# Performance work log

Hardware: AMD Instinct MI355X
Metric: run time of the kernel (lower is better)

## Reference

```python
import jax, jax.numpy as jnp
import numpy as np
from jax import lax

K_NEIGHBORS = 8  # num_neighbors
EPS_BN = 1e-5

def _bn(x, g, b, axes):
    # training-mode batch norm over `axes`, channel axis = 1
    m = jnp.mean(x, axis=axes, keepdims=True)
    v = jnp.var(x, axis=axes, keepdims=True)
    shp = [1] * x.ndim; shp[1] = x.shape[1]
    return (x - m) / jnp.sqrt(v + EPS_BN) * g.reshape(shp) + b.reshape(shp)

def _conv(x, w, b):
    y = lax.conv_general_dilated(x, w, (1, 1), 'SAME',
                                 dimension_numbers=('NCHW', 'OIHW', 'NCHW'))
    return y + b[None, :, None, None]

def setup_inputs() -> dict:
    key = jax.random.key(0)
    ks = jax.random.split(key, 20)
    B, C, H, W = 64, 200, 27, 27
    D, F, NC, HID = 64, 9, 16, 128
    inp = {
        'x': jax.random.normal(ks[0], (B, C, H, W), jnp.float32),
        'conv1_w': jax.random.normal(ks[1], (32, C, 3, 3), jnp.float32) * 0.02,
        'conv1_b': jnp.zeros((32,), jnp.float32),
        'bn1_g': jnp.ones((32,), jnp.float32), 'bn1_b': jnp.zeros((32,), jnp.float32),
        'conv2_w': jax.random.normal(ks[2], (64, 32, 3, 3), jnp.float32) * 0.05,
        'conv2_b': jnp.zeros((64,), jnp.float32),
        'bn2_g': jnp.ones((64,), jnp.float32), 'bn2_b': jnp.zeros((64,), jnp.float32),
        'conv3_w': jax.random.normal(ks[3], (D, 64, 3, 3), jnp.float32) * 0.05,
        'conv3_b': jnp.zeros((D,), jnp.float32),
        'bn3_g': jnp.ones((D,), jnp.float32), 'bn3_b': jnp.zeros((D,), jnp.float32),
        'w_self': jax.random.normal(ks[4], (D, D), jnp.float32) * (2.0 / (2 * D)) ** 0.5,
        'w_nb': jax.random.normal(ks[5], (D, D), jnp.float32) * (2.0 / (2 * D)) ** 0.5,
        'gkan_bias': jnp.zeros((D,), jnp.float32),
        'kan_a': jax.random.normal(ks[6], (D, 3), jnp.float32) * 0.1,
        'kan_b': jax.random.normal(ks[7], (D, 2), jnp.float32) * 0.1,
        'gkan_bn_g': jnp.ones((D,), jnp.float32), 'gkan_bn_b': jnp.zeros((D,), jnp.float32),
        'centers': jax.random.normal(ks[8], (D, F), jnp.float32),
        'gamma': jnp.ones((D, F), jnp.float32) * 0.5,
        'attn_w1': jax.random.normal(ks[9], (D // 4, D), jnp.float32) * 0.1,
        'attn_b1': jnp.zeros((D // 4,), jnp.float32),
        'attn_w2': jax.random.normal(ks[10], (D, D // 4), jnp.float32) * 0.1,
        'attn_b2': jnp.zeros((D,), jnp.float32),
        'fa_bn_g': jnp.ones((D,), jnp.float32), 'fa_bn_b': jnp.zeros((D,), jnp.float32),
        'fc1_w': jax.random.normal(ks[11], (HID, D), jnp.float32) * 0.1,
        'fc1_b': jnp.zeros((HID,), jnp.float32),
        'cls_bn_g': jnp.ones((HID,), jnp.float32), 'cls_bn_b': jnp.zeros((HID,), jnp.float32),
        'fc2_w': jax.random.normal(ks[12], (NC, HID), jnp.float32) * 0.1,
        'fc2_b': jnp.zeros((NC,), jnp.float32),
    }
    return inp

def _forward(x, conv1_w, conv1_b, bn1_g, bn1_b, conv2_w, conv2_b, bn2_g, bn2_b,
             conv3_w, conv3_b, bn3_g, bn3_b, w_self, w_nb, gkan_bias, kan_a, kan_b,
             gkan_bn_g, gkan_bn_b, centers, gamma, attn_w1, attn_b1, attn_w2, attn_b2,
             fa_bn_g, fa_bn_b, fc1_w, fc1_b, cls_bn_g, cls_bn_b, fc2_w, fc2_b):
    # --- CNN encoder ---
    h = jax.nn.relu(_bn(_conv(x, conv1_w, conv1_b), bn1_g, bn1_b, (0, 2, 3)))
    h = jax.nn.relu(_bn(_conv(h, conv2_w, conv2_b), bn2_g, bn2_b, (0, 2, 3)))
    h = jax.nn.relu(_bn(_conv(h, conv3_w, conv3_b), bn3_g, bn3_b, (0, 2, 3)))
    # --- tokenize: [B,D,H,W] -> [B,N,D] ---
    B, D, H, W = h.shape
    N = H * W
    t = h.reshape(B, D, N).transpose(0, 2, 1)
    # --- kNN graph (vectorized topk + scatter) ---
    xx = jnp.sum(t * t, axis=-1, keepdims=True)               # [B,N,1]
    xy = jnp.einsum('bnd,bmd->bnm', t, t)                     # [B,N,N]
    dist = jnp.maximum(xx - 2.0 * xy + xx.transpose(0, 2, 1), 0.0)
    k = min(K_NEIGHBORS + 1, N)
    _, idx = lax.top_k(-dist, k)                              # smallest-k, [B,N,k]
    adj = jnp.zeros((B, N, N), t.dtype).at[
        jnp.arange(B)[:, None, None], jnp.arange(N)[None, :, None], idx[:, :, 1:]
    ].set(1.0)
    deg = jnp.sum(adj, axis=-1) + 1e-6                        # [B,N]
    dinv = deg ** -0.5
    adj_norm = dinv[:, :, None] * adj * dinv[:, None, :] + jnp.eye(N, dtype=t.dtype)[None]
    # --- GKAN graph conv ---
    h_self = t @ w_self                                       # [B,N,D]
    h_nb = jnp.einsum('bnm,bmd->bnd', adj_norm, t @ w_nb)
    g = h_self + h_nb + gkan_bias
    g2 = g * g
    num = kan_a[:, 0] + kan_a[:, 1] * g + kan_a[:, 2] * g2
    den = 1.0 + jnp.abs(kan_b[:, 0] * g + kan_b[:, 1] * g2)
    g = num / (den + 1e-8)
    g = _bn(g.transpose(0, 2, 1), gkan_bn_g, gkan_bn_b, (0, 2)).transpose(0, 2, 1)
    # --- Fuzzy attention (RBF membership; logsumexp(log(v+1e-10)) == sum(v+1e-10)) ---
    d2 = (g[..., None] - centers[None, None]) ** 2            # [B,N,D,F]
    rbf = jnp.sum(jnp.exp(-jnp.abs(gamma)[None, None] * d2) + 1e-10, axis=-1)
    a1 = jax.nn.relu(rbf @ attn_w1.T + attn_b1)
    attn = jax.nn.sigmoid(a1 @ attn_w2.T + attn_b2)
    g = g * attn + g
    g = _bn(g.transpose(0, 2, 1), fa_bn_g, fa_bn_b, (0, 2)).transpose(0, 2, 1)
    # dropout: identity in eval
    # --- global pool + classifier ---
    p = 0.5 * jnp.mean(g, axis=1) + 0.5 * jnp.max(g, axis=1)  # [B,D]
    c = p @ fc1_w.T + fc1_b
    c = jax.nn.relu(_bn(c, cls_bn_g, cls_bn_b, (0,)))
    return c @ fc2_w.T + fc2_b

def reference(x, conv1_w, conv1_b, bn1_g, bn1_b, conv2_w, conv2_b, bn2_g, bn2_b,
              conv3_w, conv3_b, bn3_g, bn3_b, w_self, w_nb, gkan_bias, kan_a, kan_b,
              gkan_bn_g, gkan_bn_b, centers, gamma, attn_w1, attn_b1, attn_w2, attn_b2,
              fa_bn_g, fa_bn_b, fc1_w, fc1_b, cls_bn_g, cls_bn_b, fc2_w, fc2_b):
    return _forward(x, conv1_w, conv1_b, bn1_g, bn1_b, conv2_w, conv2_b, bn2_g, bn2_b,
                    conv3_w, conv3_b, bn3_g, bn3_b, w_self, w_nb, gkan_bias, kan_a, kan_b,
                    gkan_bn_g, gkan_bn_b, centers, gamma, attn_w1, attn_b1, attn_w2, attn_b2,
                    fa_bn_g, fa_bn_b, fc1_w, fc1_b, cls_bn_g, cls_bn_b, fc2_w, fc2_b)
```

## Files before the change

### kernel.cpp

```cpp
#include <hip/hip_runtime.h>
#include <math.h>

#define BATCH 64
#define NTOK  729
#define DIM   64
#define NROWS 46656

#define SROW 33
#define SCH  (29 * SROW)

template<int CIN_CHUNK, int TC, bool BN_IN>
__global__ __launch_bounds__(256) void conv3x3_v3(
    const float* __restrict__ in, const float* __restrict__ wgt,
    const float* __restrict__ scsh, float* __restrict__ outp,
    int Cin, int Cout, int cinPerSlab, int nslab)
{
  int groups = Cout / TC;
  int blocksPerB = groups * nslab;
  int b = blockIdx.x / blocksPerB;
  int rr = blockIdx.x % blocksPerB;
  int g = rr / nslab;
  int slab = rr % nslab;
  int c_begin = slab * cinPerSlab;
  int c_end = c_begin + cinPerSlab; if (c_end > Cin) c_end = Cin;

  __shared__ float s_in[CIN_CHUNK * SCH];
  __shared__ float s_w[TC * CIN_CHUNK * 12];
  __shared__ float s_sc[CIN_CHUNK];
  __shared__ float s_sh[CIN_CHUNK];

  const int tid = threadIdx.x;
  const bool active = tid < 243;
  const int py = tid / 9;
  const int px3 = (tid % 9) * 3;

  float acc[TC][3];
  #pragma unroll
  for (int t = 0; t < TC; ++t) { acc[t][0]=0.f; acc[t][1]=0.f; acc[t][2]=0.f; }

  const size_t inB = (size_t)b * Cin;

  for (int c0 = c_begin; c0 < c_end; c0 += CIN_CHUNK) {
    int ccn = c_end - c0; if (ccn > CIN_CHUNK) ccn = CIN_CHUNK;
    if (BN_IN && tid < ccn) {
      s_sc[tid] = scsh[c0 + tid];
      s_sh[tid] = scsh[Cin + c0 + tid];
    }
    __syncthreads();
    for (int i = tid; i < CIN_CHUNK * SCH; i += 256) {
      int cc = i / SCH; int r2 = i - cc * SCH; int y = r2 / SROW; int x2 = r2 - y * SROW;
      float v = 0.f;
      if (cc < ccn && y >= 1 && y <= 27 && x2 >= 1 && x2 <= 27) {
        v = in[(inB + (c0 + cc)) * 729 + (y - 1) * 27 + (x2 - 1)];
        if (BN_IN) v = fmaxf(fmaf(v, s_sc[cc], s_sh[cc]), 0.f);
      }
      s_in[i] = v;
    }
    for (int i = tid; i < TC * CIN_CHUNK * 9; i += 256) {
      int t = i / (CIN_CHUNK * 9); int r2 = i - t * CIN_CHUNK * 9;
      int cc = r2 / 9; int k = r2 - cc * 9;
      float wv = 0.f;
      if (cc < ccn) wv = wgt[((size_t)(g * TC + t) * Cin + (c0 + cc)) * 9 + k];
      s_w[(t * CIN_CHUNK + cc) * 12 + k] = wv;
    }
    __syncthreads();
    if (active) {
      #pragma unroll 1
      for (int cc = 0; cc < ccn; ++cc) {
        const float* bp = &s_in[cc * SCH + py * SROW + px3];
        float v00=bp[0],        v01=bp[1],        v02=bp[2],        v03=bp[3],        v04=bp[4];
        float v10=bp[SROW],     v11=bp[SROW+1],   v12=bp[SROW+2],   v13=bp[SROW+3],   v14=bp[SROW+4];
        float v20=bp[2*SROW],   v21=bp[2*SROW+1], v22=bp[2*SROW+2], v23=bp[2*SROW+3], v24=bp[2*SROW+4];
        #pragma unroll
        for (int t = 0; t < TC; ++t) {
          const float4 wa = *(const float4*)&s_w[(t * CIN_CHUNK + cc) * 12];
          const float4 wb = *(const float4*)&s_w[(t * CIN_CHUNK + cc) * 12 + 4];
          const float  w8 = s_w[(t * CIN_CHUNK + cc) * 12 + 8];
          acc[t][0] += wa.x*v00+wa.y*v01+wa.z*v02 + wa.w*v10+wb.x*v11+wb.y*v12 + wb.z*v20+wb.w*v21+w8*v22;
          acc[t][1] += wa.x*v01+wa.y*v02+wa.z*v03 + wa.w*v11+wb.x*v12+wb.y*v13 + wb.z*v21+wb.w*v22+w8*v23;
          acc[t][2] += wa.x*v02+wa.y*v03+wa.z*v04 + wa.w*v12+wb.x*v13+wb.y*v14 + wb.z*v22+wb.w*v23+w8*v24;
        }
      }
    }
  }
  if (active) {
    #pragma unroll
    for (int t = 0; t < TC; ++t) {
      size_t base = (((size_t)slab * BATCH + b) * Cout + (g * TC + t)) * 729 + py * 27 + px3;
      outp[base+0]=acc[t][0]; outp[base+1]=acc[t][1]; outp[base+2]=acc[t][2];
    }
  }
}

__global__ __launch_bounds__(256) void conv_reduce_stats(
    const float* __restrict__ part, const float* __restrict__ bias,
    float* __restrict__ outp, double* __restrict__ stats, int C, int nslab)
{
  int b = blockIdx.x / C;
  int c = blockIdx.x % C;
  size_t slabStride = (size_t)BATCH * C * 729;
  size_t base = ((size_t)b * C + c) * 729;
  float bv = bias[c];
  float bsum = 0.f, bsq = 0.f;
  for (int e = threadIdx.x; e < 729; e += 256) {
    float v = bv;
    for (int s = 0; s < nslab; ++s) v += part[s*slabStride + base + e];
    outp[base + e] = v;
    bsum += v; bsq += v*v;
  }
  #pragma unroll
  for (int off = 32; off > 0; off >>= 1) {
    bsum += __shfl_down(bsum, off);
    bsq  += __shfl_down(bsq, off);
  }
  __shared__ float rs[4], rq[4];
  int wid = threadIdx.x >> 6;
  if ((threadIdx.x & 63) == 0) { rs[wid] = bsum; rq[wid] = bsq; }
  __syncthreads();
  if (threadIdx.x == 0) {
    float s1 = rs[0]+rs[1]+rs[2]+rs[3];
    float q1 = rq[0]+rq[1]+rq[2]+rq[3];
    atomicAdd(&stats[c], (double)s1);
    atomicAdd(&stats[C + c], (double)q1);
  }
}

__global__ void bn_finalize(const double* __restrict__ stats,
                            const float* __restrict__ gamma, const float* __restrict__ beta,
                            float* __restrict__ scsh, int C, float invCount)
{
  int c = threadIdx.x + blockIdx.x * blockDim.x; if (c >= C) return;
  double mu = stats[c] * (double)invCount;
  double var = stats[C + c] * (double)invCount - mu * mu;
  float rstd = (float)(1.0 / sqrt(var + 1e-5));
  float sc = gamma[c] * rstd;
  scsh[c] = sc;
  scsh[C + c] = beta[c] - (float)mu * sc;
}

__global__ __launch_bounds__(256) void bn_transpose_xx(
    const float* __restrict__ c3, const float* __restrict__ scsh,
    float* __restrict__ t, float* __restrict__ xx)
{
  int lb = (blockIdx.x & 7) * 96 + (blockIdx.x >> 3);
  int b = lb / 12, nt = lb % 12, n0 = nt * 64;
  __shared__ float s[64 * 65];
  for (int i = threadIdx.x; i < 4096; i += 256) {
    int d = i >> 6, j = i & 63; int n = n0 + j;
    float v = 0.f;
    if (n < 729) {
      v = c3[((size_t)b * 64 + d) * 729 + n];
      v = fmaxf(fmaf(v, scsh[d], scsh[64 + d]), 0.f);
    }
    s[d * 65 + j] = v;
  }
  __syncthreads();
  for (int i = threadIdx.x; i < 4096; i += 256) {
    int j = i >> 6, d = i & 63; int n = n0 + j;
    if (n < 729) t[((size_t)b * 729 + n) * 64 + d] = s[d * 65 + j];
  }
  if (threadIdx.x < 64) {
    int j = threadIdx.x; int n = n0 + j;
    if (n < 729) {
      float sm = 0.f;
      #pragma unroll
      for (int d = 0; d < 64; ++d) { float v = s[d * 65 + j]; sm += v * v; }
      xx[b * 729 + n] = sm;
    }
  }
}

__global__ __launch_bounds__(256) void gemm_selfnb(
    const float* __restrict__ t, const float* __restrict__ wself,
    const float* __restrict__ wnb, float* __restrict__ hs, float* __restrict__ hw)
{
  int lb = (blockIdx.x & 7) * 96 + (blockIdx.x >> 3);
  int b = lb / 12, nt = lb % 12, n0 = nt * 64;
  __shared__ __align__(16) float s_tT[64 * 68];
  __shared__ __align__(16) float s_a[64 * 68];
  __shared__ __align__(16) float s_b[64 * 68];
  const int tid = threadIdx.x;
  for (int i = tid; i < 1024; i += 256) {
    int n = i >> 4, dq = i & 15;
    float4 v = make_float4(0.f, 0.f, 0.f, 0.f);
    if (n0 + n < 729) v = *(const float4*)&t[((size_t)b * 729 + n0 + n) * 64 + 4 * dq];
    s_tT[(4*dq+0)*68 + n] = v.x;
    s_tT[(4*dq+1)*68 + n] = v.y;
    s_tT[(4*dq+2)*68 + n] = v.z;
    s_tT[(4*dq+3)*68 + n] = v.w;
  }
  for (int i = tid; i < 1024; i += 256) {
    int d = i >> 4, jq = i & 15;
    *(float4*)&s_a[d*68 + 4*jq] = *(const float4*)&wself[d*64 + 4*jq];
    *(float4*)&s_b[d*68 + 4*jq] = *(const float4*)&wnb[d*64 + 4*jq];
  }
  __syncthreads();
  int ty = tid >> 4, tx = tid & 15;
  float acc0[4][4], acc1[4][4];
  #pragma unroll
  for (int i = 0; i < 4; ++i)
    #pragma unroll
    for (int j = 0; j < 4; ++j) { acc0[i][j] = 0.f; acc1[i][j] = 0.f; }
  #pragma unroll 8
  for (int d = 0; d < 64; ++d) {
    float4 av = *(const float4*)&s_tT[d*68 + 4*ty];
    float4 b1 = *(const float4*)&s_a[d*68 + 4*tx];
    float4 b2 = *(const float4*)&s_b[d*68 + 4*tx];
    float a[4] = {av.x, av.y, av.z, av.w};
    float u[4] = {b1.x, b1.y, b1.z, b1.w};
    float w[4] = {b2.x, b2.y, b2.z, b2.w};
    #pragma unroll
    for (int i = 0; i < 4; ++i)
      #pragma unroll
      for (int j = 0; j < 4; ++j) { acc0[i][j] += a[i]*u[j]; acc1[i][j] += a[i]*w[j]; }
  }
  #pragma unroll
  for (int i = 0; i < 4; ++i) {
    int n = n0 + 4*ty + i;
    if (n < 729) {
      size_t o = ((size_t)b * 729 + n) * 64 + 4*tx;
      *(float4*)&hs[o] = make_float4(acc0[i][0], acc0[i][1], acc0[i][2], acc0[i][3]);
      *(float4*)&hw[o] = make_float4(acc1[i][0], acc1[i][1], acc1[i][2], acc1[i][3]);
    }
  }
}

__global__ __launch_bounds__(256) void dist_topk(
    const float* __restrict__ t, const float* __restrict__ xx, int* __restrict__ nbr)
{
  int lb = (blockIdx.x & 7) * 96 + (blockIdx.x >> 3);
  int b = lb / 12, nt = lb % 12, n0 = nt * 64;
  __shared__ __align__(16) float s_nT[64 * 68];
  __shared__ __align__(16) float s_mT[64 * 68];
  __shared__ __align__(16) float s_S[64 * 68];

  const int tid = threadIdx.x;
  const int ty = tid >> 4, tx = tid & 15;
  const int r = tid & 63, q = tid >> 6;
  const int n_self = n0 + r;
  const size_t tb = (size_t)b * 729;

  float kv[8]; int ki[8];
  #pragma unroll
  for (int i = 0; i < 8; ++i) { kv[i] = 3.0e38f; ki[i] = 0x7fffffff; }

  for (int i = tid; i < 1024; i += 256) {
    int n = i >> 4, dq = i & 15;
    float4 v = make_float4(0.f, 0.f, 0.f, 0.f);
    if (n0 + n < 729) v = *(const float4*)&t[(tb + n0 + n) * 64 + 4 * dq];
    s_nT[(4*dq+0)*68 + n] = v.x;
    s_nT[(4*dq+1)*68 + n] = v.y;
    s_nT[(4*dq+2)*68 + n] = v.z;
    s_nT[(4*dq+3)*68 + n] = v.w;
  }
  for (int i = tid; i < 1024; i += 256) {
    int m = i >> 4, dq = i & 15;
    float4 v = *(const float4*)&t[(tb + m) * 64 + 4 * dq];
    s_mT[(4*dq+0)*68 + m] = v.x;
    s_mT[(4*dq+1)*68 + m] = v.y;
    s_mT[(4*dq+2)*68 + m] = v.z;
    s_mT[(4*dq+3)*68 + m] = v.w;
  }
  __syncthreads();

  for (int mt = 0; mt < 12; ++mt) {
    int m0 = mt * 64;
    float acc[4][4];
    #pragma unroll
    for (int i = 0; i < 4; ++i)
      #pragma unroll
      for (int j = 0; j < 4; ++j) acc[i][j] = 0.f;
    #pragma unroll 8
    for (int d = 0; d < 64; ++d) {
      float4 av4 = *(const float4*)&s_nT[d*68 + 4*ty];
      float4 bv4 = *(const float4*)&s_mT[d*68 + 4*tx];
      float a[4] = {av4.x, av4.y, av4.z, av4.w};
      float bb[4] = {bv4.x, bv4.y, bv4.z, bv4.w};
      #pragma unroll
      for (int i = 0; i < 4; ++i)
        #pragma unroll
        for (int j = 0; j < 4; ++j) acc[i][j] += a[i] * bb[j];
    }
    float xm[4];
    #pragma unroll
    for (int j = 0; j < 4; ++j) {
      int m = m0 + 4*tx + j;
      xm[j] = (m < 729) ? xx[b * 729 + m] : 3.0e38f;
    }
    #pragma unroll
    for (int i = 0; i < 4; ++i) {
      float4 sc = make_float4(fmaf(-2.f, acc[i][0], xm[0]), fmaf(-2.f, acc[i][1], xm[1]),
                              fmaf(-2.f, acc[i][2], xm[2]), fmaf(-2.f, acc[i][3], xm[3]));
      *(float4*)&s_S[(4*ty + i)*68 + 4*tx] = sc;
    }
    __syncthreads();
    if (mt < 11) {
      int m0n = (mt + 1) * 64;
      for (int i = tid; i < 1024; i += 256) {
        int m = i >> 4, dq = i & 15;
        float4 v = make_float4(0.f, 0.f, 0.f, 0.f);
        if (m0n + m < 729) v = *(const float4*)&t[(tb + m0n + m) * 64 + 4 * dq];
        s_mT[(4*dq+0)*68 + m] = v.x;
        s_mT[(4*dq+1)*68 + m] = v.y;
        s_mT[(4*dq+2)*68 + m] = v.z;
        s_mT[(4*dq+3)*68 + m] = v.w;
      }
    }
    #pragma unroll
    for (int c = 0; c < 4; ++c) {
      float4 s4 = *(const float4*)&s_S[r*68 + q*16 + 4*c];
      float sv[4] = {s4.x, s4.y, s4.z, s4.w};
      #pragma unroll
      for (int k = 0; k < 4; ++k) {
        int m = m0 + q*16 + 4*c + k;
        bool valid = (m < 729) && (m != n_self);
        bool lt = valid && ((sv[k] < kv[7]) || (sv[k] == kv[7] && m < ki[7]));
        if (lt) {
          float cv = sv[k]; int ci = m;
          #pragma unroll
          for (int ii = 0; ii < 8; ++ii) {
            bool less = (cv < kv[ii]) || (cv == kv[ii] && ci < ki[ii]);
            float tv = less ? kv[ii] : cv; int ti = less ? ki[ii] : ci;
            kv[ii] = less ? cv : kv[ii]; ki[ii] = less ? ci : ki[ii];
            cv = tv; ci = ti;
          }
        }
      }
    }
    __syncthreads();
  }
  float* mv = s_mT;
  int*   mi = (int*)s_nT;
  #pragma unroll
  for (int i2 = 0; i2 < 8; ++i2) { mv[r*33 + q*8 + i2] = kv[i2]; mi[r*33 + q*8 + i2] = ki[i2]; }
  __syncthreads();
  if (tid < 64) {
    int n = n0 + tid;
    if (n < 729) {
      int rb = tid * 33;
      int p0 = 0, p1 = 0, p2 = 0, p3 = 0;
      int* op = &nbr[((size_t)b * 729 + n) * 8];
      for (int o = 0; o < 8; ++o) {
        float bvv = 3.5e38f; int bii = 0x7fffffff; int bq = 0;
        {
          float v = mv[rb + 0*8 + p0]; int ii = mi[rb + 0*8 + p0];
          if (v < bvv || (v == bvv && ii < bii)) { bvv = v; bii = ii; bq = 0; }
        }
        {
          float v = mv[rb + 1*8 + p1]; int ii = mi[rb + 1*8 + p1];
          if (v < bvv || (v == bvv && ii < bii)) { bvv = v; bii = ii; bq = 1; }
        }
        {
          float v = mv[rb + 2*8 + p2]; int ii = mi[rb + 2*8 + p2];
          if (v < bvv || (v == bvv && ii < bii)) { bvv = v; bii = ii; bq = 2; }
        }
        {
          float v = mv[rb + 3*8 + p3]; int ii = mi[rb + 3*8 + p3];
          if (v < bvv || (v == bvv && ii < bii)) { bvv = v; bii = ii; bq = 3; }
        }
        p0 += (bq == 0); p1 += (bq == 1); p2 += (bq == 2); p3 += (bq == 3);
        op[o] = bii;
      }
    }
  }
}

__global__ __launch_bounds__(256) void gkan_kernel(
    const float* __restrict__ hs, const float* __restrict__ hw,
    const int* __restrict__ nbr, const float* __restrict__ bias,
    const float* __restrict__ kan_a, const float* __restrict__ kan_b,
    float* __restrict__ gpre)
{
  int row = blockIdx.x * 4 + (threadIdx.x >> 6);
  int d = threadIdx.x & 63;
  float degf = 8.0f + 1e-6f;
  float coef = 1.0f / degf;
  size_t bbase = (size_t)(row / 729) * 729;
  float v = hs[(size_t)row * 64 + d] + hw[(size_t)row * 64 + d] + bias[d];
  float nsum = 0.f;
  #pragma unroll
  for (int j = 0; j < 8; ++j) {
    int m = nbr[(size_t)row * 8 + j];
    nsum += hw[(bbase + m) * 64 + d];
  }
  v += coef * nsum;
  float a0 = kan_a[d*3], a1 = kan_a[d*3+1], a2 = kan_a[d*3+2];
  float b0 = kan_b[d*2], b1 = kan_b[d*2+1];
  float v2 = v * v;
  float num = a0 + a1*v + a2*v2;
  float den = 1.f + fabsf(b0*v + b1*v2);
  gpre[(size_t)row * 64 + d] = num / (den + 1e-8f);
}

__global__ __launch_bounds__(256) void stats_tok(
    const float* __restrict__ g, double* __restrict__ stats)
{
  int d = threadIdx.x & 63, qq = threadIdx.x >> 6;
  int r0 = blockIdx.x * 183;
  int rend = r0 + 183; if (rend > NROWS) rend = NROWS;
  float sm = 0.f, sq = 0.f;
  for (int r = r0 + qq; r < rend; r += 4) {
    float v = g[(size_t)r * 64 + d];
    sm += v; sq += v * v;
  }
  __shared__ float ls[256], lq[256];
  ls[threadIdx.x] = sm; lq[threadIdx.x] = sq;
  __syncthreads();
  if (threadIdx.x < 64) {
    sm = ls[d] + ls[64+d] + ls[128+d] + ls[192+d];
    sq = lq[d] + lq[64+d] + lq[128+d] + lq[192+d];
    atomicAdd(&stats[d], (double)sm);
    atomicAdd(&stats[64 + d], (double)sq);
  }
}

__global__ __launch_bounds__(256) void fuzzy_attn(
    const float* __restrict__ gpre, const float* __restrict__ scshG,
    const float* __restrict__ centers, const float* __restrict__ gam,
    const float* __restrict__ w1, const float* __restrict__ b1,
    const float* __restrict__ w2, const float* __restrict__ b2,
    float* __restrict__ g2)
{
  int wv = threadIdx.x >> 6, d = threadIdx.x & 63;
  int row = blockIdx.x * 4 + wv;
  __shared__ float s_rbf[4][64];
  __shared__ float s_a1[4][16];
  float v = gpre[(size_t)row * 64 + d];
  float gn = fmaf(v, scshG[d], scshG[64 + d]);
  float acc = 0.f;
  #pragma unroll
  for (int f = 0; f < 9; ++f) {
    float dc = gn - centers[d*9 + f];
    acc += expf(-fabsf(gam[d*9 + f]) * dc * dc);
  }
  s_rbf[wv][d] = acc + 9e-10f;
  __syncthreads();
  if (d < 16) {
    float a = b1[d];
    #pragma unroll 8
    for (int k = 0; k < 64; ++k) a += w1[d*64 + k] * s_rbf[wv][k];
    s_a1[wv][d] = fmaxf(a, 0.f);
  }
  __syncthreads();
  float a2 = b2[d];
  #pragma unroll
  for (int i = 0; i < 16; ++i) a2 += w2[d*16 + i] * s_a1[wv][i];
  float sig = 1.f / (1.f + expf(-a2));
  g2[(size_t)row * 64 + d] = gn * (1.f + sig);
}

__global__ __launch_bounds__(256) void pool_kernel(
    const float* __restrict__ g2, const float* __restrict__ scshF, float* __restrict__ p)
{
  int b = blockIdx.x;
  int d = threadIdx.x & 63, qq = threadIdx.x >> 6;
  float sc = scshF[d], sh = scshF[64 + d];
  float sm = 0.f, mx = -3.0e38f;
  for (int n = qq; n < 729; n += 4) {
    float v = fmaf(g2[((size_t)b * 729 + n) * 64 + d], sc, sh);
    sm += v; mx = fmaxf(mx, v);
  }
  __shared__ float ls[256], lm[256];
  ls[threadIdx.x] = sm; lm[threadIdx.x] = mx;
  __syncthreads();
  if (threadIdx.x < 64) {
    sm = ls[d] + ls[64+d] + ls[128+d] + ls[192+d];
    mx = fmaxf(fmaxf(lm[d], lm[64+d]), fmaxf(lm[128+d], lm[192+d]));
    p[b * 64 + d] = 0.5f * (sm / 729.f) + 0.5f * mx;
  }
}

__global__ __launch_bounds__(256) void classifier(
    const float* __restrict__ p, const float* __restrict__ f1w, const float* __restrict__ f1b,
    const float* __restrict__ bng, const float* __restrict__ bnb,
    const float* __restrict__ f2w, const float* __restrict__ f2b, float* __restrict__ outp)
{
  __shared__ float s_p[64 * 64];
  __shared__ float s_c[64 * 128];
  __shared__ float s_sc[128], s_sh[128];
  for (int i = threadIdx.x; i < 4096; i += 256) s_p[i] = p[i];
  __syncthreads();
  for (int o = threadIdx.x; o < 8192; o += 256) {
    int b = o >> 7, h = o & 127;
    float acc = f1b[h];
    #pragma unroll 8
    for (int d = 0; d < 64; ++d) acc += s_p[b*64 + d] * f1w[h*64 + d];
    s_c[o] = acc;
  }
  __syncthreads();
  if (threadIdx.x < 128) {
    int h = threadIdx.x;
    float sm = 0.f, sq = 0.f;
    for (int b = 0; b < 64; ++b) { float v = s_c[b*128 + h]; sm += v; sq += v*v; }
    float mu = sm / 64.f;
    float var = sq / 64.f - mu * mu;
    float rstd = rsqrtf(var + 1e-5f);
    float sc = bng[h] * rstd;
    s_sc[h] = sc; s_sh[h] = bnb[h] - mu * sc;
  }
  __syncthreads();
  for (int o = threadIdx.x; o < 1024; o += 256) {
    int b = o >> 4, j = o & 15;
    float acc = f2b[j];
    #pragma unroll 8
    for (int h = 0; h < 128; ++h) {
      float v = fmaxf(fmaf(s_c[b*128 + h], s_sc[h], s_sh[h]), 0.f);
      acc += f2w[j*128 + h] * v;
    }
    outp[o] = acc;
  }
}

extern "C" void kernel_launch(void* const* d_in, const int* in_sizes, int n_in,
                              void* d_out, int out_size, void* d_ws, size_t ws_size,
                              hipStream_t stream)
{
  const float* x      = (const float*)d_in[0];
  const float* c1w    = (const float*)d_in[1];
  const float* c1b    = (const float*)d_in[2];
  const float* bn1g   = (const float*)d_in[3];
  const float* bn1b   = (const float*)d_in[4];
  const float* c2wt   = (const float*)d_in[5];
  const float* c2b    = (const float*)d_in[6];
  const float* bn2g   = (const float*)d_in[7];
  const float* bn2b   = (const float*)d_in[8];
  const float* c3wt   = (const float*)d_in[9];
  const float* c3b    = (const float*)d_in[10];
  const float* bn3g   = (const float*)d_in[11];
  const float* bn3b   = (const float*)d_in[12];
  const float* wself  = (const float*)d_in[13];
  const float* wnb    = (const float*)d_in[14];
  const float* gbias  = (const float*)d_in[15];
  const float* kana   = (const float*)d_in[16];
  const float* kanb   = (const float*)d_in[17];
  const float* gbng   = (const float*)d_in[18];
  const float* gbnb   = (const float*)d_in[19];
  const float* cent   = (const float*)d_in[20];
  const float* gamr   = (const float*)d_in[21];
  const float* aw1    = (const float*)d_in[22];
  const float* ab1    = (const float*)d_in[23];
  const float* aw2    = (const float*)d_in[24];
  const float* ab2    = (const float*)d_in[25];
  const float* fbng   = (const float*)d_in[26];
  const float* fbnb   = (const float*)d_in[27];
  const float* f1w    = (const float*)d_in[28];
  const float* f1b    = (const float*)d_in[29];
  const float* cbng   = (const float*)d_in[30];
  const float* cbnb   = (const float*)d_in[31];
  const float* f2w    = (const float*)d_in[32];
  const float* f2b    = (const float*)d_in[33];

  char* ws = (char*)d_ws;
  float*  P     = (float*) (ws + 0);
  float*  c1    = (float*) (ws + 23887872);
  float*  c2    = (float*) (ws + 29859840);
  float*  c3    = (float*) (ws + 41803776);
  int*    nbr   = (int*)   (ws + 53747712);
  float*  xx    = (float*) (ws + 55240704);
  double* stats = (double*)(ws + 55427328);
  float*  scsh  = (float*) (ws + 55431936);
  float*  pbuf  = (float*) (ws + 55434240);
  float* hw   = P;
  float* t    = (float*)(ws + 11943936);
  float* hs   = c2;
  float* gpre = c3;
  float* g2   = t;

  hipMemsetAsync(stats, 0, 576 * sizeof(double), stream);

  const float inv = 1.0f / 46656.0f;

  conv3x3_v3<8,8,false><<<dim3(1024), dim3(256), 0, stream>>>(
      x,  c1w, nullptr, P, 200, 32, 50, 4);
  conv_reduce_stats<<<dim3(2048), dim3(256), 0, stream>>>(P, c1b, c1, stats, 32, 4);
  bn_finalize<<<dim3(1), dim3(32), 0, stream>>>(stats, bn1g, bn1b, scsh, 32, inv);
  conv3x3_v3<8,8,true><<<dim3(1024), dim3(256), 0, stream>>>(
      c1, c2wt, scsh, P, 32, 64, 16, 2);
  conv_reduce_stats<<<dim3(4096), dim3(256), 0, stream>>>(P, c2b, c2, stats + 64, 64, 2);
  bn_finalize<<<dim3(1), dim3(64), 0, stream>>>(stats + 64, bn2g, bn2b, scsh + 64, 64, inv);
  conv3x3_v3<8,8,true><<<dim3(1024), dim3(256), 0, stream>>>(
      c2, c3wt, scsh + 64, P, 64, 64, 32, 2);
  conv_reduce_stats<<<dim3(4096), dim3(256), 0, stream>>>(P, c3b, c3, stats + 192, 64, 2);
  bn_finalize<<<dim3(1), dim3(64), 0, stream>>>(stats + 192, bn3g, bn3b, scsh + 192, 64, inv);
  bn_transpose_xx<<<dim3(768), dim3(256), 0, stream>>>(c3, scsh + 192, t, xx);
  gemm_selfnb<<<dim3(768), dim3(256), 0, stream>>>(t, wself, wnb, hs, hw);
  dist_topk<<<dim3(768), dim3(256), 0, stream>>>(t, xx, nbr);
  gkan_kernel<<<dim3(11664), dim3(256), 0, stream>>>(hs, hw, nbr, gbias, kana, kanb, gpre);
  stats_tok<<<dim3(256), dim3(256), 0, stream>>>(gpre, stats + 320);
  bn_finalize<<<dim3(1), dim3(64), 0, stream>>>(stats + 320, gbng, gbnb, scsh + 320, 64, inv);
  fuzzy_attn<<<dim3(11664), dim3(256), 0, stream>>>(gpre, scsh + 320, cent, gamr, aw1, ab1, aw2, ab2, g2);
  stats_tok<<<dim3(256), dim3(256), 0, stream>>>(g2, stats + 448);
  bn_finalize<<<dim3(1), dim3(64), 0, stream>>>(stats + 448, fbng, fbnb, scsh + 448, 64, inv);
  pool_kernel<<<dim3(64), dim3(256), 0, stream>>>(g2, scsh + 448, pbuf);
  classifier<<<dim3(1), dim3(256), 0, stream>>>(pbuf, f1w, f1b, cbng, cbnb, f2w, f2b, (float*)d_out);
}
```

Before: 994.4 us.

## Compute two output rows per thread and 16 channels per block in conv3x3

The 3x3 conv kernel now has each block cover 16 output channels, split into two groups of 128 threads with 8 channels each. Each thread computes a 2-row by 3-column output tile, so four input rows loaded from shared memory serve six outputs per channel, up from three rows for three outputs. The grid is halved to 512 blocks and the shared input buffer is padded by one row for the extra read. In exchange, register pressure rises (48 accumulators) and 2 of every 128 threads sit idle, which may lower occupancy.

Result: faster. 885.6 us (-10.9%).

```diff
diff --git a/kernel.cpp b/kernel.cpp
--- a/kernel.cpp
+++ b/kernel.cpp
@@ -9,34 +9,40 @@
 #define SROW 33
 #define SCH  (29 * SROW)
 
-template<int CIN_CHUNK, int TC, bool BN_IN>
-__global__ __launch_bounds__(256) void conv3x3_v3(
+template<int CIN_CHUNK, bool BN_IN>
+__global__ __launch_bounds__(256) void conv3x3_v4(
     const float* __restrict__ in, const float* __restrict__ wgt,
     const float* __restrict__ scsh, float* __restrict__ outp,
     int Cin, int Cout, int cinPerSlab, int nslab)
 {
-  int groups = Cout / TC;
-  int blocksPerB = groups * nslab;
+  int bigGroups = Cout / 16;
+  int blocksPerB = bigGroups * nslab;
   int b = blockIdx.x / blocksPerB;
   int rr = blockIdx.x % blocksPerB;
-  int g = rr / nslab;
+  int bg = rr / nslab;
   int slab = rr % nslab;
   int c_begin = slab * cinPerSlab;
   int c_end = c_begin + cinPerSlab; if (c_end > Cin) c_end = Cin;
 
-  __shared__ float s_in[CIN_CHUNK * SCH];
-  __shared__ float s_w[TC * CIN_CHUNK * 12];
+  __shared__ float s_in[CIN_CHUNK * SCH + SROW];
+  __shared__ float s_w[16 * CIN_CHUNK * 12];
   __shared__ float s_sc[CIN_CHUNK];
   __shared__ float s_sh[CIN_CHUNK];
 
   const int tid = threadIdx.x;
-  const bool active = tid < 243;
-  const int py = tid / 9;
-  const int px3 = (tid % 9) * 3;
-
-  float acc[TC][3];
-  #pragma unroll
-  for (int t = 0; t < TC; ++t) { acc[t][0]=0.f; acc[t][1]=0.f; acc[t][2]=0.f; }
+  const int grp = tid >> 7;
+  const int idx = tid & 127;
+  const bool active = idx < 126;
+  const int rp = idx / 9;
+  const int py = 2 * rp;
+  const int px3 = (idx % 9) * 3;
+  const bool row2ok = (py + 1) < 27;
+
+  float acc[8][2][3];
+  #pragma unroll
+  for (int t = 0; t < 8; ++t)
+    #pragma unroll
+    for (int rI = 0; rI < 2; ++rI) { acc[t][rI][0]=0.f; acc[t][rI][1]=0.f; acc[t][rI][2]=0.f; }
 
   const size_t inB = (size_t)b * Cin;
 
@@ -56,11 +62,11 @@
       }
       s_in[i] = v;
     }
-    for (int i = tid; i < TC * CIN_CHUNK * 9; i += 256) {
+    for (int i = tid; i < 16 * CIN_CHUNK * 9; i += 256) {
       int t = i / (CIN_CHUNK * 9); int r2 = i - t * CIN_CHUNK * 9;
       int cc = r2 / 9; int k = r2 - cc * 9;
       float wv = 0.f;
-      if (cc < ccn) wv = wgt[((size_t)(g * TC + t) * Cin + (c0 + cc)) * 9 + k];
+      if (cc < ccn) wv = wgt[((size_t)(bg * 16 + t) * Cin + (c0 + cc)) * 9 + k];
       s_w[(t * CIN_CHUNK + cc) * 12 + k] = wv;
     }
     __syncthreads();
@@ -68,26 +74,41 @@
       #pragma unroll 1
       for (int cc = 0; cc < ccn; ++cc) {
         const float* bp = &s_in[cc * SCH + py * SROW + px3];
-        float v00=bp[0],        v01=bp[1],        v02=bp[2],        v03=bp[3],        v04=bp[4];
-        float v10=bp[SROW],     v11=bp[SROW+1],   v12=bp[SROW+2],   v13=bp[SROW+3],   v14=bp[SROW+4];
-        float v20=bp[2*SROW],   v21=bp[2*SROW+1], v22=bp[2*SROW+2], v23=bp[2*SROW+3], v24=bp[2*SROW+4];
+        float r0[5], r1[5], r2[5], r3[5];
         #pragma unroll
-        for (int t = 0; t < TC; ++t) {
-          const float4 wa = *(const float4*)&s_w[(t * CIN_CHUNK + cc) * 12];
-          const float4 wb = *(const float4*)&s_w[(t * CIN_CHUNK + cc) * 12 + 4];
-          const float  w8 = s_w[(t * CIN_CHUNK + cc) * 12 + 8];
-          acc[t][0] += wa.x*v00+wa.y*v01+wa.z*v02 + wa.w*v10+wb.x*v11+wb.y*v12 + wb.z*v20+wb.w*v21+w8*v22;
-          acc[t][1] += wa.x*v01+wa.y*v02+wa.z*v03 + wa.w*v11+wb.x*v12+wb.y*v13 + wb.z*v21+wb.w*v22+w8*v23;
-          acc[t][2] += wa.x*v02+wa.y*v03+wa.z*v04 + wa.w*v12+wb.x*v13+wb.y*v14 + wb.z*v22+wb.w*v23+w8*v24;
+        for (int j = 0; j < 5; ++j) {
+          r0[j] = bp[j];
+          r1[j] = bp[SROW + j];
+          r2[j] = bp[2*SROW + j];
+          r3[j] = bp[3*SROW + j];
+        }
+        #pragma unroll
+        for (int t = 0; t < 8; ++t) {
+          const int wb = ((grp * 8 + t) * CIN_CHUNK + cc) * 12;
+          const float4 wa = *(const float4*)&s_w[wb];
+          const float4 wc = *(const float4*)&s_w[wb + 4];
+          const float  w8 = s_w[wb + 8];
+          #pragma unroll
+          for (int p = 0; p < 3; ++p) {
+            acc[t][0][p] += wa.x*r0[p]+wa.y*r0[p+1]+wa.z*r0[p+2]
+                          + wa.w*r1[p]+wc.x*r1[p+1]+wc.y*r1[p+2]
+                          + wc.z*r2[p]+wc.w*r2[p+1]+w8*r2[p+2];
+            acc[t][1][p] += wa.x*r1[p]+wa.y*r1[p+1]+wa.z*r1[p+2]
+                          + wa.w*r2[p]+wc.x*r2[p+1]+wc.y*r2[p+2]
+                          + wc.z*r3[p]+wc.w*r3[p+1]+w8*r3[p+2];
+          }
         }
       }
     }
   }
   if (active) {
     #pragma unroll
-    for (int t = 0; t < TC; ++t) {
-      size_t base = (((size_t)slab * BATCH + b) * Cout + (g * TC + t)) * 729 + py * 27 + px3;
-      outp[base+0]=acc[t][0]; outp[base+1]=acc[t][1]; outp[base+2]=acc[t][2];
+    for (int t = 0; t < 8; ++t) {
+      size_t base = (((size_t)slab * BATCH + b) * Cout + (bg * 16 + grp * 8 + t)) * 729 + py * 27 + px3;
+      outp[base+0]=acc[t][0][0]; outp[base+1]=acc[t][0][1]; outp[base+2]=acc[t][0][2];
+      if (row2ok) {
+        outp[base+27]=acc[t][1][0]; outp[base+28]=acc[t][1][1]; outp[base+29]=acc[t][1][2];
+      }
     }
   }
 }
@@ -570,15 +591,15 @@
 
   const float inv = 1.0f / 46656.0f;
 
-  conv3x3_v3<8,8,false><<<dim3(1024), dim3(256), 0, stream>>>(
+  conv3x3_v4<8,false><<<dim3(512), dim3(256), 0, stream>>>(
       x,  c1w, nullptr, P, 200, 32, 50, 4);
   conv_reduce_stats<<<dim3(2048), dim3(256), 0, stream>>>(P, c1b, c1, stats, 32, 4);
   bn_finalize<<<dim3(1), dim3(32), 0, stream>>>(stats, bn1g, bn1b, scsh, 32, inv);
-  conv3x3_v3<8,8,true><<<dim3(1024), dim3(256), 0, stream>>>(
+  conv3x3_v4<8,true><<<dim3(512), dim3(256), 0, stream>>>(
       c1, c2wt, scsh, P, 32, 64, 16, 2);
   conv_reduce_stats<<<dim3(4096), dim3(256), 0, stream>>>(P, c2b, c2, stats + 64, 64, 2);
   bn_finalize<<<dim3(1), dim3(64), 0, stream>>>(stats + 64, bn2g, bn2b, scsh + 64, 64, inv);
-  conv3x3_v3<8,8,true><<<dim3(1024), dim3(256), 0, stream>>>(
+  conv3x3_v4<8,true><<<dim3(512), dim3(256), 0, stream>>>(
       c2, c3wt, scsh + 64, P, 64, 64, 32, 2);
   conv_reduce_stats<<<dim3(4096), dim3(256), 0, stream>>>(P, c3b, c3, stats + 192, 64, 2);
   bn_finalize<<<dim3(1), dim3(64), 0, stream>>>(stats + 192, bn3g, bn3b, scsh + 192, 64, inv);
```
